# Kernel tuning notes

Measured on AMD Instinct MI355X. Metric: run time of the kernel, lower is better.

The kernel has to match this reference:

```python
import jax, jax.numpy as jnp
import numpy as np

N_NODES = 100000
N_EDGES = 3200000
IN_FEATURES = 128
OUT_FEATURES = 32


def setup_inputs() -> dict:
    key = jax.random.key(0)
    k_x, k_w, k_src, k_dst, k_ew = jax.random.split(key, 5)
    x = jax.random.normal(k_x, (N_NODES, IN_FEATURES), dtype=jnp.float32)
    W = jax.random.normal(k_w, (IN_FEATURES, OUT_FEATURES), dtype=jnp.float32) * (1.0 / np.sqrt(IN_FEATURES))
    edge_src = jax.random.randint(k_src, (N_EDGES,), 0, N_NODES, dtype=jnp.int32)
    edge_dst = jax.random.randint(k_dst, (N_EDGES,), 0, N_NODES, dtype=jnp.int32)
    edge_weight = jax.random.uniform(k_ew, (N_EDGES,), dtype=jnp.float32)
    return {"x": x, "W": W, "edge_src": edge_src, "edge_dst": edge_dst, "edge_weight": edge_weight}


def reference(x, W, edge_src, edge_dst, edge_weight):
    # GCNConv.forward: h = linear(x) (no bias), then out = sparse.mm(A_hat, h)
    h = x @ W                                   # [N, out]
    # SpMM as gather -> weight -> segment-sum over destination nodes.
    msgs = edge_weight[:, None] * h[edge_src]   # [E, out]
    out = jax.ops.segment_sum(msgs, edge_dst, num_segments=N_NODES)  # [N, out]
    return out
```

## Files before the change

kernel.cpp:

```cpp
#include <hip/hip_runtime.h>
#include <hip/hip_bf16.h>

#define IN_F 128
#define OUT_F 32
#define BSHIFT 7
#define NPB 128
#define BCHUNK 4096
#define BIN_THREADS 1024
#define GAT_THREADS 512
#define TILE 2048
#define MAXBIN 1024
#define CAP 5120

static __device__ inline unsigned short f2bf_rne(float f) {
    unsigned u = __float_as_uint(f);
    unsigned r = u + 0x7FFF + ((u >> 16) & 1);
    return (unsigned short)(r >> 16);
}

__global__ void gcn_gemm_h(const float* __restrict__ x, const float* __restrict__ W,
                           unsigned short* __restrict__ h, int n_rows,
                           int* __restrict__ gcur, int nb)
{
    __shared__ float Wl[IN_F * OUT_F];
    const int tid = threadIdx.x;
    if (blockIdx.x == 0)
        for (int i = tid; i < nb; i += 256) gcur[i] = i * CAP;

    const float4* W4 = (const float4*)W;
    float4* Wl4 = (float4*)Wl;
    #pragma unroll
    for (int i = 0; i < 4; ++i)
        Wl4[tid + i * 256] = W4[tid + i * 256];
    __syncthreads();

    const int c4   = tid & 7;
    const int rloc = tid >> 3;
    const int row  = blockIdx.x * 32 + rloc;
    if (row >= n_rows) return;

    const float4* xr = (const float4*)(x + (size_t)row * IN_F);
    float4 acc = {0.f, 0.f, 0.f, 0.f};
    #pragma unroll
    for (int k4 = 0; k4 < IN_F / 4; ++k4) {
        const float4 xv = xr[k4];
        #pragma unroll
        for (int j = 0; j < 4; ++j) {
            const int k = k4 * 4 + j;
            const float4 wv = *(const float4*)(&Wl[k * OUT_F + c4 * 4]);
            const float xs = (&xv.x)[j];
            acc.x += xs * wv.x;
            acc.y += xs * wv.y;
            acc.z += xs * wv.z;
            acc.w += xs * wv.w;
        }
    }
    ushort4 o = { f2bf_rne(acc.x), f2bf_rne(acc.y), f2bf_rne(acc.z), f2bf_rne(acc.w) };
    *(ushort4*)(&h[(size_t)row * OUT_F + c4 * 4]) = o;
}

__global__ __launch_bounds__(BIN_THREADS)
void gcn_bin(const int* __restrict__ esrc, const int* __restrict__ edst,
             const float* __restrict__ ew, int* __restrict__ gcur,
             int2* __restrict__ recs, int n_edges, int nb)
{
    __shared__ int2 sorted[BCHUNK];
    __shared__ unsigned short binOf[BCHUNK];
    __shared__ int hist[MAXBIN];
    __shared__ int cursor[MAXBIN];
    __shared__ int gbase[MAXBIN];
    __shared__ int wpart[16];
    __shared__ int wpre[16];

    const int tid = threadIdx.x;
    const int k   = blockIdx.x;
    const int base  = k * BCHUNK;
    const int count = min(BCHUNK, n_edges - base);
    const int i0    = tid * 4;
    const bool full = (i0 + 3 < count);

    int4 d4 = {0, 0, 0, 0};
    int4 s4 = {0, 0, 0, 0};
    float4 w4 = {0.f, 0.f, 0.f, 0.f};
    if (full) {
        d4 = ((const int4*)(edst + base))[tid];
        s4 = ((const int4*)(esrc + base))[tid];
        w4 = ((const float4*)(ew + base))[tid];
    } else {
        if (i0     < count) { d4.x = edst[base + i0];     s4.x = esrc[base + i0];     w4.x = ew[base + i0]; }
        if (i0 + 1 < count) { d4.y = edst[base + i0 + 1]; s4.y = esrc[base + i0 + 1]; w4.y = ew[base + i0 + 1]; }
        if (i0 + 2 < count) { d4.z = edst[base + i0 + 2]; s4.z = esrc[base + i0 + 2]; w4.z = ew[base + i0 + 2]; }
    }

    for (int i = tid; i < nb; i += BIN_THREADS) hist[i] = 0;
    __syncthreads();

    if (full) {
        atomicAdd(&hist[d4.x >> BSHIFT], 1);
        atomicAdd(&hist[d4.y >> BSHIFT], 1);
        atomicAdd(&hist[d4.z >> BSHIFT], 1);
        atomicAdd(&hist[d4.w >> BSHIFT], 1);
    } else {
        if (i0     < count) atomicAdd(&hist[d4.x >> BSHIFT], 1);
        if (i0 + 1 < count) atomicAdd(&hist[d4.y >> BSHIFT], 1);
        if (i0 + 2 < count) atomicAdd(&hist[d4.z >> BSHIFT], 1);
    }
    __syncthreads();

    const int v = (tid < nb) ? hist[tid] : 0;
    int sc = v;
    #pragma unroll
    for (int off = 1; off < 64; off <<= 1) {
        const int t = __shfl_up(sc, off, 64);
        if ((tid & 63) >= off) sc += t;
    }
    if ((tid & 63) == 63) wpart[tid >> 6] = sc;
    __syncthreads();
    if (tid < 16) {
        const int pv = wpart[tid];
        int ps = pv;
        #pragma unroll
        for (int off = 1; off < 16; off <<= 1) {
            const int t = __shfl_up(ps, off, 64);
            if (tid >= off) ps += t;
        }
        wpre[tid] = ps - pv;
    }
    __syncthreads();
    if (tid < nb) {
        const int beg = sc - v + wpre[tid >> 6];
        cursor[tid] = beg;
        int gb = 0;
        if (v > 0) gb = atomicAdd(&gcur[tid], v);
        gbase[tid] = gb - beg;
    }
    __syncthreads();

    if (full) {
        #pragma unroll
        for (int j = 0; j < 4; ++j) {
            const int d  = (&d4.x)[j];
            const int bk = d >> BSHIFT;
            const int pos = atomicAdd(&cursor[bk], 1);
            sorted[pos] = make_int2((&s4.x)[j] | ((d & (NPB - 1)) << 17),
                                    __float_as_int((&w4.x)[j]));
            binOf[pos]  = (unsigned short)bk;
        }
    } else {
        #pragma unroll
        for (int j = 0; j < 4; ++j) {
            if (i0 + j < count) {
                const int d  = (&d4.x)[j];
                const int bk = d >> BSHIFT;
                const int pos = atomicAdd(&cursor[bk], 1);
                sorted[pos] = make_int2((&s4.x)[j] | ((d & (NPB - 1)) << 17),
                                        __float_as_int((&w4.x)[j]));
                binOf[pos]  = (unsigned short)bk;
            }
        }
    }
    __syncthreads();

    if (full) {
        #pragma unroll
        for (int j = 0; j < 4; ++j) {
            const int i = i0 + j;
            recs[gbase[binOf[i]] + i] = sorted[i];
        }
    } else {
        #pragma unroll
        for (int j = 0; j < 4; ++j) {
            const int i = i0 + j;
            if (i < count) recs[gbase[binOf[i]] + i] = sorted[i];
        }
    }
}

__global__ __launch_bounds__(GAT_THREADS)
void gcn_sort_gather(const unsigned short* __restrict__ h,
                     const int2* __restrict__ recs,
                     const int* __restrict__ gcur,
                     float* __restrict__ out, int n_nodes)
{
    __shared__ int2 sbuf[TILE];
    __shared__ int2 sorted[TILE];
    __shared__ int hist[NPB];
    __shared__ int nbeg[NPB];
    __shared__ int cursor[NPB];
    __shared__ int wpart[2];

    const int b   = blockIdx.x;
    const int tid = threadIdx.x;
    const int s   = b * CAP;
    const int cnt = gcur[b] - s;
    const int grp = tid >> 2;
    const int q   = tid & 3;
    const size_t hoff = (size_t)(q << 3);

    float a0 = 0.f, a1 = 0.f, a2 = 0.f, a3 = 0.f;
    float a4 = 0.f, a5 = 0.f, a6 = 0.f, a7 = 0.f;

    for (int t0 = 0; t0 < cnt; t0 += TILE) {
        const int tc = min(TILE, cnt - t0);
        __syncthreads();
        if (tid < NPB) hist[tid] = 0;
        __syncthreads();
        for (int i = tid; i < tc; i += GAT_THREADS) {
            const int2 r = recs[s + t0 + i];
            sbuf[i] = r;
            atomicAdd(&hist[(r.x >> 17) & (NPB - 1)], 1);
        }
        __syncthreads();

        const int v = (tid < NPB) ? hist[tid] : 0;
        int sc = v;
        #pragma unroll
        for (int off = 1; off < 64; off <<= 1) {
            const int t = __shfl_up(sc, off, 64);
            if ((tid & 63) >= off) sc += t;
        }
        if (tid < NPB && (tid & 63) == 63) wpart[tid >> 6] = sc;
        __syncthreads();
        if (tid < NPB) {
            const int beg = sc - v + ((tid >= 64) ? wpart[0] : 0);
            nbeg[tid]   = beg;
            cursor[tid] = beg;
        }
        __syncthreads();

        for (int i = tid; i < tc; i += GAT_THREADS) {
            const int2 r = sbuf[i];
            const int pos = atomicAdd(&cursor[(r.x >> 17) & (NPB - 1)], 1);
            sorted[pos] = r;
        }
        __syncthreads();

        {
            int i = nbeg[grp];
            const int e = i + hist[grp];
            for (; i + 4 <= e; i += 4) {
                const int2 r0 = sorted[i];
                const int2 r1 = sorted[i + 1];
                const int2 r2 = sorted[i + 2];
                const int2 r3 = sorted[i + 3];
                const uint4 v0 = *(const uint4*)(h + (((size_t)(r0.x & 0x1FFFF)) << 5) + hoff);
                const uint4 v1 = *(const uint4*)(h + (((size_t)(r1.x & 0x1FFFF)) << 5) + hoff);
                const uint4 v2 = *(const uint4*)(h + (((size_t)(r2.x & 0x1FFFF)) << 5) + hoff);
                const uint4 v3 = *(const uint4*)(h + (((size_t)(r3.x & 0x1FFFF)) << 5) + hoff);
                const float w0 = __int_as_float(r0.y);
                const float w1 = __int_as_float(r1.y);
                const float w2 = __int_as_float(r2.y);
                const float w3 = __int_as_float(r3.y);
                a0 += w0 * __uint_as_float(v0.x << 16);
                a1 += w0 * __uint_as_float(v0.x & 0xFFFF0000u);
                a2 += w0 * __uint_as_float(v0.y << 16);
                a3 += w0 * __uint_as_float(v0.y & 0xFFFF0000u);
                a4 += w0 * __uint_as_float(v0.z << 16);
                a5 += w0 * __uint_as_float(v0.z & 0xFFFF0000u);
                a6 += w0 * __uint_as_float(v0.w << 16);
                a7 += w0 * __uint_as_float(v0.w & 0xFFFF0000u);
                a0 += w1 * __uint_as_float(v1.x << 16);
                a1 += w1 * __uint_as_float(v1.x & 0xFFFF0000u);
                a2 += w1 * __uint_as_float(v1.y << 16);
                a3 += w1 * __uint_as_float(v1.y & 0xFFFF0000u);
                a4 += w1 * __uint_as_float(v1.z << 16);
                a5 += w1 * __uint_as_float(v1.z & 0xFFFF0000u);
                a6 += w1 * __uint_as_float(v1.w << 16);
                a7 += w1 * __uint_as_float(v1.w & 0xFFFF0000u);
                a0 += w2 * __uint_as_float(v2.x << 16);
                a1 += w2 * __uint_as_float(v2.x & 0xFFFF0000u);
                a2 += w2 * __uint_as_float(v2.y << 16);
                a3 += w2 * __uint_as_float(v2.y & 0xFFFF0000u);
                a4 += w2 * __uint_as_float(v2.z << 16);
                a5 += w2 * __uint_as_float(v2.z & 0xFFFF0000u);
                a6 += w2 * __uint_as_float(v2.w << 16);
                a7 += w2 * __uint_as_float(v2.w & 0xFFFF0000u);
                a0 += w3 * __uint_as_float(v3.x << 16);
                a1 += w3 * __uint_as_float(v3.x & 0xFFFF0000u);
                a2 += w3 * __uint_as_float(v3.y << 16);
                a3 += w3 * __uint_as_float(v3.y & 0xFFFF0000u);
                a4 += w3 * __uint_as_float(v3.z << 16);
                a5 += w3 * __uint_as_float(v3.z & 0xFFFF0000u);
                a6 += w3 * __uint_as_float(v3.w << 16);
                a7 += w3 * __uint_as_float(v3.w & 0xFFFF0000u);
            }
            for (; i < e; ++i) {
                const int2 r = sorted[i];
                const uint4 hv = *(const uint4*)(h + (((size_t)(r.x & 0x1FFFF)) << 5) + hoff);
                const float w = __int_as_float(r.y);
                a0 += w * __uint_as_float(hv.x << 16);
                a1 += w * __uint_as_float(hv.x & 0xFFFF0000u);
                a2 += w * __uint_as_float(hv.y << 16);
                a3 += w * __uint_as_float(hv.y & 0xFFFF0000u);
                a4 += w * __uint_as_float(hv.z << 16);
                a5 += w * __uint_as_float(hv.z & 0xFFFF0000u);
                a6 += w * __uint_as_float(hv.w << 16);
                a7 += w * __uint_as_float(hv.w & 0xFFFF0000u);
            }
        }
    }

    const int node = (b << BSHIFT) + grp;
    if (node < n_nodes) {
        float* op = out + ((size_t)node << 5) + (q << 3);
        float4 o0 = { a0, a1, a2, a3 };
        float4 o1 = { a4, a5, a6, a7 };
        *(float4*)(op)     = o0;
        *(float4*)(op + 4) = o1;
    }
}

__global__ void gcn_fused_fallback(const float* __restrict__ x, const float* __restrict__ W,
                                   const int* __restrict__ esrc,
                                   const int* __restrict__ edst,
                                   const float* __restrict__ ew,
                                   float* __restrict__ out,
                                   long long total_units)
{
    __shared__ float Wl[IN_F * OUT_F];
    const int tid = threadIdx.x;
    const float4* W4 = (const float4*)W;
    float4* Wl4 = (float4*)Wl;
    #pragma unroll
    for (int i = 0; i < 4; ++i)
        Wl4[tid + i * 256] = W4[tid + i * 256];
    __syncthreads();

    long long u = (long long)blockIdx.x * blockDim.x + threadIdx.x;
    if (u >= total_units) return;
    const int e = (int)(u >> 5);
    const int c = (int)(u & 31);
    const int s  = esrc[e];
    const int d  = edst[e];
    const float w = ew[e];

    const float4* xr = (const float4*)(x + (size_t)s * IN_F);
    float acc = 0.f;
    #pragma unroll
    for (int k4 = 0; k4 < IN_F / 4; ++k4) {
        const float4 xv = xr[k4];
        acc += xv.x * Wl[(k4 * 4 + 0) * OUT_F + c];
        acc += xv.y * Wl[(k4 * 4 + 1) * OUT_F + c];
        acc += xv.z * Wl[(k4 * 4 + 2) * OUT_F + c];
        acc += xv.w * Wl[(k4 * 4 + 3) * OUT_F + c];
    }
    atomicAdd(out + (size_t)d * OUT_F + c, w * acc);
}

static inline size_t align_up(size_t v, size_t a) { return (v + a - 1) & ~(a - 1); }

extern "C" void kernel_launch(void* const* d_in, const int* in_sizes, int n_in,
                              void* d_out, int out_size, void* d_ws, size_t ws_size,
                              hipStream_t stream)
{
    const float* x  = (const float*)d_in[0];
    const float* W  = (const float*)d_in[1];
    const int* esrc = (const int*)d_in[2];
    const int* edst = (const int*)d_in[3];
    const float* ew = (const float*)d_in[4];
    float* out = (float*)d_out;

    const int n_nodes = in_sizes[0] / IN_F;
    const int n_edges = in_sizes[2];

    const int nb       = (n_nodes + NPB - 1) >> BSHIFT;
    const int n_chunks = (n_edges + BCHUNK - 1) / BCHUNK;
    const int avg_per_bucket = n_edges / nb;

    const size_t h_bytes    = align_up((size_t)n_nodes * OUT_F * sizeof(unsigned short), 256);
    const size_t cur_bytes  = align_up((size_t)nb * sizeof(int), 256);
    const size_t recs_bytes = align_up((size_t)nb * CAP * sizeof(int2) + 16, 256);
    const size_t need = h_bytes + cur_bytes + recs_bytes;

    if (ws_size >= need && nb <= MAXBIN && avg_per_bucket + 16 * 64 < CAP) {
        char* p = (char*)d_ws;
        unsigned short* h = (unsigned short*)p;  p += h_bytes;
        int* gcur     = (int*)p;                 p += cur_bytes;
        int2* recs    = (int2*)p;

        const int gemm_blocks = (n_nodes + 31) / 32;
        gcn_gemm_h<<<gemm_blocks, 256, 0, stream>>>(x, W, h, n_nodes, gcur, nb);

        gcn_bin<<<n_chunks, BIN_THREADS, 0, stream>>>(esrc, edst, ew, gcur,
                                                      recs, n_edges, nb);
        gcn_sort_gather<<<nb, GAT_THREADS, 0, stream>>>(h, recs, gcur, out, n_nodes);
    } else {
        hipMemsetAsync(d_out, 0, (size_t)out_size * sizeof(float), stream);
        const long long total_units = (long long)n_edges * 32;
        const int fblocks = (int)((total_units + 255) / 256);
        gcn_fused_fallback<<<fblocks, 256, 0, stream>>>(x, W, esrc, edst, ew, out, total_units);
    }
}
```

Baseline: 94.15 us.

## Scatter binned edges directly to global memory, dropping the local sort stage

The binning kernel no longer sorts each chunk into shared memory with a block-wide prefix scan before writing out. Each bin's global slot is reserved once per block, and every edge then takes a shared-memory atomic cursor and writes straight to its global record position. The global counters now hold per-bin counts instead of absolute offsets. This removes the scan, two barriers and a lot of shared memory, which may raise occupancy, but the global writes become scattered rather than grouped by bin, so coalescing may suffer.

```diff
diff --git a/kernel.cpp b/kernel.cpp
--- a/kernel.cpp
+++ b/kernel.cpp
@@ -25,7 +25,7 @@
     __shared__ float Wl[IN_F * OUT_F];
     const int tid = threadIdx.x;
     if (blockIdx.x == 0)
-        for (int i = tid; i < nb; i += 256) gcur[i] = i * CAP;
+        for (int i = tid; i < nb; i += 256) gcur[i] = 0;
 
     const float4* W4 = (const float4*)W;
     float4* Wl4 = (float4*)Wl;
@@ -64,13 +64,8 @@
              const float* __restrict__ ew, int* __restrict__ gcur,
              int2* __restrict__ recs, int n_edges, int nb)
 {
-    __shared__ int2 sorted[BCHUNK];
-    __shared__ unsigned short binOf[BCHUNK];
     __shared__ int hist[MAXBIN];
-    __shared__ int cursor[MAXBIN];
-    __shared__ int gbase[MAXBIN];
-    __shared__ int wpart[16];
-    __shared__ int wpre[16];
+    __shared__ int cursorG[MAXBIN];
 
     const int tid = threadIdx.x;
     const int k   = blockIdx.x;
@@ -107,32 +102,10 @@
     }
     __syncthreads();
 
-    const int v = (tid < nb) ? hist[tid] : 0;
-    int sc = v;
-    #pragma unroll
-    for (int off = 1; off < 64; off <<= 1) {
-        const int t = __shfl_up(sc, off, 64);
-        if ((tid & 63) >= off) sc += t;
-    }
-    if ((tid & 63) == 63) wpart[tid >> 6] = sc;
-    __syncthreads();
-    if (tid < 16) {
-        const int pv = wpart[tid];
-        int ps = pv;
-        #pragma unroll
-        for (int off = 1; off < 16; off <<= 1) {
-            const int t = __shfl_up(ps, off, 64);
-            if (tid >= off) ps += t;
-        }
-        wpre[tid] = ps - pv;
-    }
-    __syncthreads();
     if (tid < nb) {
-        const int beg = sc - v + wpre[tid >> 6];
-        cursor[tid] = beg;
-        int gb = 0;
-        if (v > 0) gb = atomicAdd(&gcur[tid], v);
-        gbase[tid] = gb - beg;
+        const int v = hist[tid];
+        if (v > 0)
+            cursorG[tid] = tid * CAP + atomicAdd(&gcur[tid], v);
     }
     __syncthreads();
 
@@ -141,10 +114,9 @@
         for (int j = 0; j < 4; ++j) {
             const int d  = (&d4.x)[j];
             const int bk = d >> BSHIFT;
-            const int pos = atomicAdd(&cursor[bk], 1);
-            sorted[pos] = make_int2((&s4.x)[j] | ((d & (NPB - 1)) << 17),
-                                    __float_as_int((&w4.x)[j]));
-            binOf[pos]  = (unsigned short)bk;
+            const int pos = atomicAdd(&cursorG[bk], 1);
+            recs[pos] = make_int2((&s4.x)[j] | ((d & (NPB - 1)) << 17),
+                                  __float_as_int((&w4.x)[j]));
         }
     } else {
         #pragma unroll
@@ -152,26 +124,10 @@
             if (i0 + j < count) {
                 const int d  = (&d4.x)[j];
                 const int bk = d >> BSHIFT;
-                const int pos = atomicAdd(&cursor[bk], 1);
-                sorted[pos] = make_int2((&s4.x)[j] | ((d & (NPB - 1)) << 17),
-                                        __float_as_int((&w4.x)[j]));
-                binOf[pos]  = (unsigned short)bk;
+                const int pos = atomicAdd(&cursorG[bk], 1);
+                recs[pos] = make_int2((&s4.x)[j] | ((d & (NPB - 1)) << 17),
+                                      __float_as_int((&w4.x)[j]));
             }
-        }
-    }
-    __syncthreads();
-
-    if (full) {
-        #pragma unroll
-        for (int j = 0; j < 4; ++j) {
-            const int i = i0 + j;
-            recs[gbase[binOf[i]] + i] = sorted[i];
-        }
-    } else {
-        #pragma unroll
-        for (int j = 0; j < 4; ++j) {
-            const int i = i0 + j;
-            if (i < count) recs[gbase[binOf[i]] + i] = sorted[i];
         }
     }
 }
@@ -192,7 +148,7 @@
     const int b   = blockIdx.x;
     const int tid = threadIdx.x;
     const int s   = b * CAP;
-    const int cnt = gcur[b] - s;
+    const int cnt = gcur[b];
     const int grp = tid >> 2;
     const int q   = tid & 3;
     const size_t hoff = (size_t)(q << 3);
```

Measured after the change: 95.32 us. Within noise of the previous version (+1.2%).
